# Kernel tuning notes

Hardware: AMD Instinct MI355X
Metric: run time of the kernel (lower is better)

## Reference

```python
import jax, jax.numpy as jnp
import numpy as np

N = 50000      # nodes
F_IN = 500     # in_channels
MID = 64       # mid_layer_channel
H = 2          # heads
OUT = 40       # out_channels
E = 800000     # edges per order
ORDER = 3
NEG_SLOPE = 0.2


def _gat(x, edge_index, W, a_src, a_dst, b, concat):
    # PyG-style GATConv (eval mode, dropout off), with self loops.
    n = x.shape[0]
    heads, ch = a_src.shape
    h = (x @ W).reshape(n, heads, ch)                    # [N,H,C]
    loop = jnp.arange(n)
    src = jnp.concatenate([edge_index[0], loop])
    dst = jnp.concatenate([edge_index[1], loop])
    al_s = jnp.sum(h * a_src, axis=-1)                   # [N,H]
    al_d = jnp.sum(h * a_dst, axis=-1)                   # [N,H]
    e = jax.nn.leaky_relu(al_s[src] + al_d[dst], NEG_SLOPE)   # [Etot,H]
    m = jax.ops.segment_max(e, dst, num_segments=n)      # softmax over incoming edges per dst
    ex = jnp.exp(e - m[dst])
    den = jax.ops.segment_sum(ex, dst, num_segments=n)
    alpha = ex / (den[dst] + 1e-16)
    out = jax.ops.segment_sum(alpha[:, :, None] * h[src], dst, num_segments=n)  # [N,H,C]
    if concat:
        return out.reshape(n, heads * ch) + b
    return out.mean(axis=1) + b


def _aggr(states, Wmix, wfin):
    # NOrderAggrConv (depth=2): mix order states with [order,order] weights + ELU,
    # then reduce to a single state with a learned [order] combination.
    h = jnp.stack(states, axis=1)                        # [N,order,C]
    h = jax.nn.elu(jnp.einsum('nkc,kj->njc', h, Wmix))
    return jnp.einsum('nkc,k->nc', h, wfin)


def setup_inputs():
    key = jax.random.key(0)
    ks = jax.random.split(key, 40)
    d = {}
    d['node_feature'] = jax.random.normal(ks[0], (N, F_IN), jnp.float32)
    for o in range(ORDER):
        d[f'adj{o}'] = jax.random.randint(ks[1 + o], (2, E), 0, N)
    i = 4
    s = 0.05
    layer_dims = [(F_IN, MID, H * MID), (MID * H, OUT, OUT)]
    for l, (fin, c, bdim) in enumerate(layer_dims):
        for o in range(ORDER):
            d[f'W_{l}_{o}'] = jax.random.normal(ks[i], (fin, H * c), jnp.float32) * s; i += 1
            d[f'as_{l}_{o}'] = jax.random.normal(ks[i], (H, c), jnp.float32) * s; i += 1
            d[f'ad_{l}_{o}'] = jax.random.normal(ks[i], (H, c), jnp.float32) * s; i += 1
            d[f'b_{l}_{o}'] = jnp.zeros((bdim,), jnp.float32)
    for l in range(2):
        d[f'agg{l}_W'] = jax.random.normal(ks[i], (ORDER, ORDER), jnp.float32) * 0.5; i += 1
        d[f'agg{l}_w'] = jnp.full((ORDER,), 1.0 / ORDER, jnp.float32)
    return d


def reference(node_feature, adj0, adj1, adj2,
              W_0_0, as_0_0, ad_0_0, b_0_0,
              W_0_1, as_0_1, ad_0_1, b_0_1,
              W_0_2, as_0_2, ad_0_2, b_0_2,
              W_1_0, as_1_0, ad_1_0, b_1_0,
              W_1_1, as_1_1, ad_1_1, b_1_1,
              W_1_2, as_1_2, ad_1_2, b_1_2,
              agg0_W, agg0_w, agg1_W, agg1_w):
    adjs = (adj0, adj1, adj2)
    p0 = ((W_0_0, as_0_0, ad_0_0, b_0_0),
          (W_0_1, as_0_1, ad_0_1, b_0_1),
          (W_0_2, as_0_2, ad_0_2, b_0_2))
    p1 = ((W_1_0, as_1_0, ad_1_0, b_1_0),
          (W_1_1, as_1_1, ad_1_1, b_1_1),
          (W_1_2, as_1_2, ad_1_2, b_1_2))
    aggs = ((agg0_W, agg0_w), (agg1_W, agg1_w))
    x = node_feature  # eval mode: dropout is identity
    for l, params in enumerate((p0, p1)):
        concat = (l == 0)
        states = [jax.nn.elu(_gat(x, adjs[o], *params[o], concat)) for o in range(ORDER)]
        x = _aggr(states, *aggs[l])
    return jax.nn.log_softmax(x, axis=1)
```

## Files before the change

kernel.cpp:

```cpp
#include <hip/hip_runtime.h>
#include <cstdint>
#include <cstddef>
#include <math.h>


typedef __attribute__((ext_vector_type(8))) short short8;
typedef __attribute__((ext_vector_type(4))) float f32x4;
typedef __attribute__((ext_vector_type(2))) float f32x2;

struct P3f { const float* p[3]; };
struct P3c { const int* p[3]; };

__device__ __forceinline__ float leakyf(float x) { return x > 0.f ? x : 0.2f * x; }
__device__ __forceinline__ float eluf(float x)   { return x > 0.f ? x : expm1f(x); }

__device__ __forceinline__ unsigned short bf16r(float x) {
  unsigned int u = __float_as_uint(x);
  u += 0x7fffu + ((u >> 16) & 1u);
  return (unsigned short)(u >> 16);
}
__device__ __forceinline__ float bflo(unsigned int u) { return __uint_as_float(u << 16); }
__device__ __forceinline__ float bfhi(unsigned int u) { return __uint_as_float(u & 0xffff0000u); }

__device__ __forceinline__ void bf8_fma2(uint4 q, float xx, f32x2* a) {
  f32x2 v0 = {bflo(q.x), bfhi(q.x)};
  f32x2 v1 = {bflo(q.y), bfhi(q.y)};
  f32x2 v2 = {bflo(q.z), bfhi(q.z)};
  f32x2 v3 = {bflo(q.w), bfhi(q.w)};
  a[0] += xx * v0;
  a[1] += xx * v1;
  a[2] += xx * v2;
  a[3] += xx * v3;
}

__global__ __launch_bounds__(256) void zero_int_kernel(int* p, int n) {
  int i = blockIdx.x * blockDim.x + threadIdx.x;
  if (i < n) p[i] = 0;
}

__global__ __launch_bounds__(256) void convA_kernel(const float* __restrict__ A,
    unsigned short* __restrict__ Ab, int M, int K, int Kpad) {
  int i = blockIdx.x * blockDim.x + threadIdx.x;
  int row = i >> 6;
  int koff = (i & 63) * 8;
  if (row >= M) return;
  const float* ap = A + (size_t)row * K;
  unsigned short v[8];
  if (koff + 8 <= K) {
    float4 q0 = ((const float4*)(ap + koff))[0];
    float4 q1 = ((const float4*)(ap + koff))[1];
    v[0] = bf16r(q0.x); v[1] = bf16r(q0.y); v[2] = bf16r(q0.z); v[3] = bf16r(q0.w);
    v[4] = bf16r(q1.x); v[5] = bf16r(q1.y); v[6] = bf16r(q1.z); v[7] = bf16r(q1.w);
  } else {
#pragma unroll
    for (int k = 0; k < 8; ++k)
      v[k] = (koff + k < K) ? bf16r(ap[koff + k]) : (unsigned short)0;
  }
  *(uint4*)(Ab + (size_t)row * Kpad + koff) = *(const uint4*)v;
}

__global__ __launch_bounds__(256) void count3_kernel(P3c adj, int* __restrict__ cntb,
    int* __restrict__ posb, int E, int N) {
  int i = blockIdx.x * blockDim.x + threadIdx.x;
  int o = blockIdx.y;
  if (i < E) {
    int d = adj.p[o][E + i];
    posb[(size_t)o * E + i] = atomicAdd(&cntb[o * N + d], 1);
  }
}

#define SCAN_T 256
#define SCAN_VPT 8
#define SCAN_TILE 2048

__global__ __launch_bounds__(SCAN_T) void scan1_kernel(const int* __restrict__ cntb,
    int* __restrict__ rowptrb, int* __restrict__ bsums, int N) {
  __shared__ int lds[SCAN_T];
  const int o = blockIdx.y;
  const int* cnt = cntb + o * N;
  int* rowptr = rowptrb + o * (N + 1);
  int t = threadIdx.x;
  int base = blockIdx.x * SCAN_TILE + t * SCAN_VPT;
  int v[SCAN_VPT];
  int s = 0;
#pragma unroll
  for (int i = 0; i < SCAN_VPT; ++i) {
    int idx = base + i;
    int x = (idx < N) ? cnt[idx] : 0;
    s += x;
    v[i] = s;
  }
  lds[t] = s;
  __syncthreads();
  for (int off = 1; off < SCAN_T; off <<= 1) {
    int add = (t >= off) ? lds[t - off] : 0;
    __syncthreads();
    lds[t] += add;
    __syncthreads();
  }
  int excl = (t > 0) ? lds[t - 1] : 0;
#pragma unroll
  for (int i = 0; i < SCAN_VPT; ++i) {
    int idx = base + i;
    if (idx < N) rowptr[idx + 1] = excl + v[i];
  }
  if (t == SCAN_T - 1) bsums[o * 64 + blockIdx.x] = lds[t];
}

__global__ void scan2_kernel(int* bsums, int nb, int* rowptrb, int N) {
  if (threadIdx.x == 0 && blockIdx.x == 0) {
    for (int o = 0; o < 3; ++o) {
      int run = 0;
      for (int i = 0; i < nb; ++i) {
        int x = bsums[o * 64 + i];
        bsums[o * 64 + i] = run;
        run += x;
      }
      rowptrb[o * (N + 1)] = 0;
    }
  }
}

__global__ __launch_bounds__(256) void scan3_kernel(int* __restrict__ rowptrb,
    const int* __restrict__ bsums, int N) {
  int idx = blockIdx.x * blockDim.x + threadIdx.x;
  int o = blockIdx.y;
  if (idx < N) rowptrb[o * (N + 1) + idx + 1] += bsums[o * 64 + idx / SCAN_TILE];
}

__global__ __launch_bounds__(256) void fill3_kernel(P3c adj,
    const int* __restrict__ rowptrb, const int* __restrict__ posb,
    int* __restrict__ colvb, int E, int N) {
  int i = blockIdx.x * blockDim.x + threadIdx.x;
  int o = blockIdx.y;
  if (i < E) {
    const int* a = adj.p[o];
    int d = a[E + i];
    int pos = posb[(size_t)o * E + i];
    colvb[(size_t)o * E + rowptrb[o * (N + 1) + d] + pos] = a[i];
  }
}

__global__ __launch_bounds__(256) void alpha3_kernel(const int* __restrict__ rowptrB,
    const int* __restrict__ colvB, const float2* __restrict__ alsB,
    const float2* __restrict__ aldB, float2* __restrict__ alphB, int N, int E) {
  int w = blockIdx.x * blockDim.x + threadIdx.x;
  int o = blockIdx.y;
  if (w >= N) return;
  const int* rowptr = rowptrB + o * (N + 1);
  const int* colv = colvB + (size_t)o * E;
  const float2* als = alsB + (size_t)o * N;
  const float2 b = (aldB + (size_t)o * N)[w];
  float2* alph = alphB + (size_t)o * E;
  const int beg = rowptr[w], end = rowptr[w + 1];
  for (int j = beg; j < end; ++j) {
    int s = colv[j];
    float2 a = als[s];
    alph[j] = make_float2(__expf(leakyf(a.x + b.x)), __expf(leakyf(a.y + b.y)));
  }
}

__global__ __launch_bounds__(256) void conv_bt3_kernel(P3f W,
    unsigned short* __restrict__ BtB, int K, int NC, int Kpad) {
  int n = blockIdx.y;
  int o = blockIdx.z;
  int k = blockIdx.x * 256 + threadIdx.x;
  if (k >= Kpad) return;
  float v = (k < K) ? W.p[o][(size_t)k * NC + n] : 0.f;
  BtB[(size_t)o * NC * Kpad + (size_t)n * Kpad + k] = bf16r(v);
}

#define GBM 128
#define LDSTRIDE 40

template<int NT>
__device__ __forceinline__ void gemm_body(int m0, int o, int t,
    const unsigned short* __restrict__ Ab, const unsigned short* __restrict__ BtB,
    P3f asp, P3f adp, unsigned short* __restrict__ CbB,
    float2* __restrict__ alsB, float2* __restrict__ aldB, int M, int Kpad,
    unsigned short* As, unsigned short* Bs) {
  constexpr int NC = NT * 16;
  constexpr int CH = NT * 8;
  const int wave = t >> 6, lane = t & 63;
  const int quad = lane >> 4, l16 = lane & 15;
  const unsigned short* Bt = BtB + (size_t)o * NC * Kpad;
  unsigned short* Cb = CbB + (size_t)o * M * NC;
  float2* al_s = alsB + (size_t)o * M;
  float2* al_d = aldB + (size_t)o * M;
  const float* a_src = asp.p[o];
  const float* a_dst = adp.p[o];

  f32x4 acc[2][NT];
#pragma unroll
  for (int i = 0; i < 2; ++i)
#pragma unroll
    for (int j = 0; j < NT; ++j) acc[i][j] = (f32x4){0.f, 0.f, 0.f, 0.f};

  const int arow = t >> 1;
  const int akoff = (t & 1) * 16;
  const int gm = m0 + arow;
  const unsigned short* arowp = Ab + (size_t)gm * Kpad;
  const unsigned short* browp = Bt + (size_t)arow * Kpad;

  for (int k0 = 0; k0 < Kpad; k0 += 32) {
    if (k0) __syncthreads();
    const int kb = k0 + akoff;
    {
      uint4 q0 = {0, 0, 0, 0}, q1 = {0, 0, 0, 0};
      if (gm < M) {
        const uint4* p = (const uint4*)(arowp + kb);
        q0 = p[0]; q1 = p[1];
      }
      short8* dst = (short8*)&As[arow * LDSTRIDE + akoff];
      union { uint4 q; short8 s; } c0, c1;
      c0.q = q0; c1.q = q1;
      dst[0] = c0.s;
      dst[1] = c1.s;
    }
    if (arow < NC) {
      const uint4* p = (const uint4*)(browp + kb);
      uint4 q0 = p[0], q1 = p[1];
      short8* dst = (short8*)&Bs[arow * LDSTRIDE + akoff];
      union { uint4 q; short8 s; } c0, c1;
      c0.q = q0; c1.q = q1;
      dst[0] = c0.s;
      dst[1] = c1.s;
    }
    __syncthreads();
    short8 af[2];
#pragma unroll
    for (int rt = 0; rt < 2; ++rt)
      af[rt] = *(const short8*)&As[(wave * 32 + rt * 16 + l16) * LDSTRIDE + quad * 8];
    short8 bfv[NT];
#pragma unroll
    for (int ct = 0; ct < NT; ++ct)
      bfv[ct] = *(const short8*)&Bs[(ct * 16 + l16) * LDSTRIDE + quad * 8];
#pragma unroll
    for (int rt = 0; rt < 2; ++rt)
#pragma unroll
      for (int ct = 0; ct < NT; ++ct)
        acc[rt][ct] = __builtin_amdgcn_mfma_f32_16x16x32_bf16(af[rt], bfv[ct],
                                                              acc[rt][ct], 0, 0, 0);
  }
  float asv[NT], adv[NT];
#pragma unroll
  for (int ct = 0; ct < NT; ++ct) {
    int col = ct * 16 + l16;
    asv[ct] = a_src[col];
    adv[ct] = a_dst[col];
  }
#pragma unroll
  for (int rt = 0; rt < 2; ++rt) {
    int gr0 = m0 + wave * 32 + rt * 16 + quad * 4;
#pragma unroll
    for (int r = 0; r < 4; ++r) {
      int gr = gr0 + r;
      float ps0 = 0.f, ps1 = 0.f, pd0 = 0.f, pd1 = 0.f;
#pragma unroll
      for (int ct = 0; ct < NT; ++ct) {
        int col = ct * 16 + l16;
        float v = acc[rt][ct][r];
        if (gr < M) Cb[(size_t)gr * NC + col] = bf16r(v);
        if (col < CH) { ps0 += v * asv[ct]; pd0 += v * adv[ct]; }
        else          { ps1 += v * asv[ct]; pd1 += v * adv[ct]; }
      }
#pragma unroll
      for (int off = 1; off < 16; off <<= 1) {
        ps0 += __shfl_xor(ps0, off, 64);
        ps1 += __shfl_xor(ps1, off, 64);
        pd0 += __shfl_xor(pd0, off, 64);
        pd1 += __shfl_xor(pd1, off, 64);
      }
      if (l16 == 0 && gr < M) {
        al_s[gr] = make_float2(ps0, ps1);
        al_d[gr] = make_float2(pd0, pd1);
      }
    }
  }
}

template<int NT>
__global__ __launch_bounds__(256) void mfma_gemm_kernel(
    const unsigned short* __restrict__ Ab, const unsigned short* __restrict__ BtB,
    P3f asp, P3f adp, unsigned short* __restrict__ CbB,
    float2* __restrict__ alsB, float2* __restrict__ aldB, int M, int Kpad) {
  __shared__ unsigned short As[GBM * LDSTRIDE];
  __shared__ unsigned short Bs[NT * 16 * LDSTRIDE];
  gemm_body<NT>(blockIdx.x * GBM, blockIdx.y, threadIdx.x,
                Ab, BtB, asp, adp, CbB, alsB, aldB, M, Kpad, As, Bs);
}

__global__ __launch_bounds__(256) void gemm0_count_kernel(
    const unsigned short* __restrict__ Ab, const unsigned short* __restrict__ BtB,
    P3f asp, P3f adp, unsigned short* __restrict__ CbB,
    float2* __restrict__ alsB, float2* __restrict__ aldB, int M, int Kpad,
    P3c adj, int* __restrict__ cntb, int* __restrict__ posb, int E, int N,
    int nbG) {
  __shared__ unsigned short As[GBM * LDSTRIDE];
  __shared__ unsigned short Bs[128 * LDSTRIDE];
  const int x = blockIdx.x;
  const int o = blockIdx.y;
  const int gx = x / 9;
  const int rem = x - gx * 9;
  if (rem == 0 && gx < nbG) {
    gemm_body<8>(gx * GBM, o, threadIdx.x,
                 Ab, BtB, asp, adp, CbB, alsB, aldB, M, Kpad, As, Bs);
  } else {
    int nG = (x + 8) / 9;
    if (nG > nbG) nG = nbG;
    const int c = x - nG;
    const int i = c * 256 + threadIdx.x;
    if (i < E) {
      int d = adj.p[o][E + i];
      posb[(size_t)o * E + i] = atomicAdd(&cntb[o * N + d], 1);
    }
  }
}

template<int C, int CONCAT>
__global__ __launch_bounds__(256) void gat_slot4_kernel(
    const unsigned short* __restrict__ hB, const float2* __restrict__ alsB,
    const float2* __restrict__ aldB, const int* __restrict__ rowptrB,
    const int* __restrict__ colvB, const float2* __restrict__ alphB,
    P3f biasp, unsigned short* __restrict__ outB, int N, int E) {
  constexpr int HC = 2 * C;
  constexpr int FLd = HC / 8;
  constexpr int HB = C / 8;
  constexpr int OW = CONCAT ? HC : C;
  const int o = blockIdx.y;
  const unsigned short* h = hB + (size_t)o * N * HC;
  const float2* al_s = alsB + (size_t)o * N;
  const float2* al_d = aldB + (size_t)o * N;
  const int* rowptr = rowptrB + o * (N + 1);
  const int* colv = colvB + (size_t)o * E;
  const float2* alph = alphB + (size_t)o * E;
  const float* bias = biasp.p[o];
  unsigned short* out = outB + (size_t)o * N * OW;

  const int gw = (blockIdx.x * blockDim.x + threadIdx.x) >> 6;
  const int lane = threadIdx.x & 63;
  const int slot = lane >> 4;
  const int f4 = lane & 15;
  const int w = gw * 4 + slot;
  if (gw * 4 >= N) return;
  const bool vn = w < N;
  const int wc = vn ? w : N - 1;
  const bool hl = f4 < FLd;

  const int beg = rowptr[wc];
  const int deg = vn ? (rowptr[wc + 1] - beg) : 0;
  int md = deg;
  md = max(md, __shfl_xor(md, 32, 64));
  md = max(md, __shfl_xor(md, 16, 64));

  const float2 ad = al_d[wc];
  const float2 asf = al_s[wc];
  const float xs0 = __expf(leakyf(asf.x + ad.x));
  const float xs1 = __expf(leakyf(asf.y + ad.y));
  float dp0 = xs0, dp1 = xs1;

  f32x2 acc[4] = {}, acc2[4] = {};
  if (hl) {
    uint4 q = ((const uint4*)(h + (size_t)wc * HC))[f4];
    bf8_fma2(q, (f4 < HB) ? xs0 : xs1, acc);
  }

  const float2 z2 = make_float2(0.f, 0.f);
  for (int t = 0; t < md; t += 4) {
    const int j0 = beg + t;
    const bool v0 = t < deg;
    const bool v1 = t + 1 < deg;
    const bool v2 = t + 2 < deg;
    const bool v3 = t + 3 < deg;
    const int s0 = v0 ? colv[j0] : 0;
    const int s1 = v1 ? colv[j0 + 1] : 0;
    const int s2 = v2 ? colv[j0 + 2] : 0;
    const int s3 = v3 ? colv[j0 + 3] : 0;
    const float2 a0 = v0 ? alph[j0] : z2;
    const float2 a1 = v1 ? alph[j0 + 1] : z2;
    const float2 a2 = v2 ? alph[j0 + 2] : z2;
    const float2 a3 = v3 ? alph[j0 + 3] : z2;
    uint4 q0 = make_uint4(0, 0, 0, 0), q1 = q0, q2 = q0, q3 = q0;
    if (v0 && hl) q0 = ((const uint4*)(h + (size_t)s0 * HC))[f4];
    if (v1 && hl) q1 = ((const uint4*)(h + (size_t)s1 * HC))[f4];
    if (v2 && hl) q2 = ((const uint4*)(h + (size_t)s2 * HC))[f4];
    if (v3 && hl) q3 = ((const uint4*)(h + (size_t)s3 * HC))[f4];
    dp0 += (a0.x + a1.x) + (a2.x + a3.x);
    dp1 += (a0.y + a1.y) + (a2.y + a3.y);
    if (v0 && hl) bf8_fma2(q0, (f4 < HB) ? a0.x : a0.y, acc);
    if (v1 && hl) bf8_fma2(q1, (f4 < HB) ? a1.x : a1.y, acc2);
    if (v2 && hl) bf8_fma2(q2, (f4 < HB) ? a2.x : a2.y, acc);
    if (v3 && hl) bf8_fma2(q3, (f4 < HB) ? a3.x : a3.y, acc2);
  }
#pragma unroll
  for (int i = 0; i < 4; ++i) acc[i] += acc2[i];

  const float inv0 = 1.f / (dp0 + 1e-16f), inv1 = 1.f / (dp1 + 1e-16f);
  if (CONCAT) {
    if (vn && hl) {
      const float xx = (f4 < HB) ? inv0 : inv1;
      const float* bp = bias + f4 * 8;
      unsigned int pk[4];
#pragma unroll
      for (int i = 0; i < 4; ++i) {
        unsigned short lo = bf16r(eluf(acc[i][0] * xx + bp[2 * i]));
        unsigned short hi = bf16r(eluf(acc[i][1] * xx + bp[2 * i + 1]));
        pk[i] = (unsigned int)lo | ((unsigned int)hi << 16);
      }
      ((uint4*)(out + (size_t)w * OW + f4 * 8))[0] = make_uint4(pk[0], pk[1], pk[2], pk[3]);
    }
  } else {
    float p[8];
#pragma unroll
    for (int i = 0; i < 4; ++i) {
      p[2 * i]     = __shfl(acc[i][0], lane + HB, 64);
      p[2 * i + 1] = __shfl(acc[i][1], lane + HB, 64);
    }
    if (vn && f4 < HB) {
      const float* bp = bias + f4 * 8;
      unsigned int pk[4];
#pragma unroll
      for (int i = 0; i < 4; ++i) {
        float v0 = 0.5f * (acc[i][0] * inv0 + p[2 * i] * inv1) + bp[2 * i];
        float v1 = 0.5f * (acc[i][1] * inv0 + p[2 * i + 1] * inv1) + bp[2 * i + 1];
        pk[i] = (unsigned int)bf16r(eluf(v0)) | ((unsigned int)bf16r(eluf(v1)) << 16);
      }
      ((uint4*)(out + (size_t)w * OW + f4 * 8))[0] = make_uint4(pk[0], pk[1], pk[2], pk[3]);
    }
  }
}

template<int BF16OUT>
__global__ __launch_bounds__(256) void mixb_kernel(const unsigned short* __restrict__ sb,
    const float* __restrict__ Wm, const float* __restrict__ wf,
    void* __restrict__ out, int perU) {
  int i = blockIdx.x * blockDim.x + threadIdx.x;
  if (i >= perU) return;
  const unsigned int* sp = (const unsigned int*)sb;
  unsigned int u0 = sp[i];
  unsigned int u1 = sp[perU + i];
  unsigned int u2 = sp[2 * perU + i];
  float a0 = bflo(u0), a1 = bfhi(u0);
  float b0 = bflo(u1), b1 = bfhi(u1);
  float c0 = bflo(u2), c1 = bfhi(u2);
  float r0 = 0.f, r1 = 0.f;
#pragma unroll
  for (int j = 0; j < 3; ++j) {
    float w0 = Wm[j], w1 = Wm[3 + j], w2 = Wm[6 + j], wj = wf[j];
    r0 += wj * eluf(a0 * w0 + b0 * w1 + c0 * w2);
    r1 += wj * eluf(a1 * w0 + b1 * w1 + c1 * w2);
  }
  if (BF16OUT) {
    ((unsigned int*)out)[i] = (unsigned int)bf16r(r0) | ((unsigned int)bf16r(r1) << 16);
  } else {
    ((float2*)out)[i] = make_float2(r0, r1);
  }
}

__global__ __launch_bounds__(256) void log_softmax_kernel(const float* __restrict__ x,
    float* __restrict__ out, int N, int C) {
  int w = (blockIdx.x * blockDim.x + threadIdx.x) >> 6;
  int lane = threadIdx.x & 63;
  if (w >= N) return;
  float v = (lane < C) ? x[(size_t)w * C + lane] : -INFINITY;
  float mx = v;
#pragma unroll
  for (int off = 1; off < 64; off <<= 1) mx = fmaxf(mx, __shfl_xor(mx, off, 64));
  float ex = (lane < C) ? expf(v - mx) : 0.f;
  float s = ex;
#pragma unroll
  for (int off = 1; off < 64; off <<= 1) s += __shfl_xor(s, off, 64);
  if (lane < C) out[(size_t)w * C + lane] = v - mx - logf(s);
}

extern "C" void kernel_launch(void* const* d_in, const int* in_sizes, int n_in,
                              void* d_out, int out_size, void* d_ws, size_t ws_size,
                              hipStream_t stream) {
  const int F_IN = 500;
  const int N = in_sizes[0] / F_IN;
  const int E = in_sizes[1] / 2;
  const int HC0 = 128;
  const int HC1 = 80;
  const int C1 = 40;
  const int K0pad = 512, K1pad = 128;

  const float* x0 = (const float*)d_in[0];
  P3c adj;
  adj.p[0] = (const int*)d_in[1];
  adj.p[1] = (const int*)d_in[2];
  adj.p[2] = (const int*)d_in[3];
  P3f W0p, as0p, ad0p, b0p, W1p, as1p, ad1p, b1p;
  for (int o = 0; o < 3; ++o) {
    W0p.p[o]  = (const float*)d_in[4 + 4 * o + 0];
    as0p.p[o] = (const float*)d_in[4 + 4 * o + 1];
    ad0p.p[o] = (const float*)d_in[4 + 4 * o + 2];
    b0p.p[o]  = (const float*)d_in[4 + 4 * o + 3];
    W1p.p[o]  = (const float*)d_in[16 + 4 * o + 0];
    as1p.p[o] = (const float*)d_in[16 + 4 * o + 1];
    ad1p.p[o] = (const float*)d_in[16 + 4 * o + 2];
    b1p.p[o]  = (const float*)d_in[16 + 4 * o + 3];
  }
  const float* agg0W = (const float*)d_in[28];
  const float* agg0w = (const float*)d_in[29];
  const float* agg1W = (const float*)d_in[30];
  const float* agg1w = (const float*)d_in[31];

  char* ws = (char*)d_ws;
  size_t off = 0;
  auto alloc = [&](size_t bytes) -> void* {
    off = (off + 255) & ~(size_t)255;
    void* p = ws + off;
    off += bytes;
    return p;
  };
  int* rowptrb = (int*)alloc((size_t)3 * (N + 1) * 4);
  int* colvb   = (int*)alloc((size_t)3 * E * 4);
  int* cntb    = (int*)alloc((size_t)3 * N * 4);
  int* bsums   = (int*)alloc(3 * 64 * 4);
  unsigned short* x0b = (unsigned short*)alloc((size_t)N * K0pad * 2);
  unsigned short* hB  = (unsigned short*)alloc((size_t)3 * N * HC0 * 2);
  unsigned short* stB = (unsigned short*)alloc((size_t)3 * N * HC0 * 2);
  float* x2 = (float*)alloc((size_t)N * C1 * 4);
  float2* alsB = (float2*)alloc((size_t)3 * N * 8);
  float2* aldB = (float2*)alloc((size_t)3 * N * 8);
  unsigned short* Bt0B = (unsigned short*)alloc((size_t)3 * HC0 * K0pad * 2);
  unsigned short* Bt1B = (unsigned short*)alloc((size_t)3 * HC1 * K1pad * 2);
  float2* alphb = (float2*)x0b;
  int* posb = (int*)stB;
  (void)ws_size;

  const int TB = 256;
  const int nbE = (E + TB - 1) / TB;
  const int nbN = (N + TB - 1) / TB;
  const int scanBlocks = (N + SCAN_TILE - 1) / SCAN_TILE;
  const int gemmBlocks = (N + GBM - 1) / GBM;
  const int slot4Blocks = (int)(((size_t)((N + 3) / 4) * 64 + TB - 1) / TB);
  const int lsBlocks = (int)(((size_t)N * 64 + TB - 1) / TB);

  convA_kernel<<<(int)(((size_t)N * 64 + TB - 1) / TB), TB, 0, stream>>>(
      x0, x0b, N, F_IN, K0pad);
  conv_bt3_kernel<<<dim3((K0pad + 255) / 256, HC0, 3), TB, 0, stream>>>(W0p, Bt0B, F_IN, HC0, K0pad);
  conv_bt3_kernel<<<dim3((K1pad + 255) / 256, HC1, 3), TB, 0, stream>>>(W1p, Bt1B, HC0, HC1, K1pad);

  zero_int_kernel<<<(3 * N + TB - 1) / TB, TB, 0, stream>>>(cntb, 3 * N);
  if (8 * gemmBlocks >= nbE) {
    gemm0_count_kernel<<<dim3(gemmBlocks * 9, 3), TB, 0, stream>>>(
        x0b, Bt0B, as0p, ad0p, hB, alsB, aldB, N, K0pad,
        adj, cntb, posb, E, N, gemmBlocks);
  } else {
    count3_kernel<<<dim3(nbE, 3), TB, 0, stream>>>(adj, cntb, posb, E, N);
    mfma_gemm_kernel<8><<<dim3(gemmBlocks, 3), TB, 0, stream>>>(
        x0b, Bt0B, as0p, ad0p, hB, alsB, aldB, N, K0pad);
  }

  scan1_kernel<<<dim3(scanBlocks, 3), SCAN_T, 0, stream>>>(cntb, rowptrb, bsums, N);
  scan2_kernel<<<1, 64, 0, stream>>>(bsums, scanBlocks, rowptrb, N);
  scan3_kernel<<<dim3(nbN, 3), TB, 0, stream>>>(rowptrb, bsums, N);
  fill3_kernel<<<dim3(nbE, 3), TB, 0, stream>>>(adj, rowptrb, posb, colvb, E, N);

  alpha3_kernel<<<dim3(nbN, 3), TB, 0, stream>>>(rowptrb, colvb, alsB, aldB, alphb, N, E);
  gat_slot4_kernel<64, 1><<<dim3(slot4Blocks, 3), TB, 0, stream>>>(
      hB, alsB, aldB, rowptrb, colvb, alphb, b0p, stB, N, E);
  mixb_kernel<1><<<((N * HC0 / 2) + TB - 1) / TB, TB, 0, stream>>>(
      stB, agg0W, agg0w, stB, N * HC0 / 2);

  mfma_gemm_kernel<5><<<dim3(gemmBlocks, 3), TB, 0, stream>>>(
      stB, Bt1B, as1p, ad1p, hB, alsB, aldB, N, K1pad);
  alpha3_kernel<<<dim3(nbN, 3), TB, 0, stream>>>(rowptrb, colvb, alsB, aldB, alphb, N, E);
  gat_slot4_kernel<40, 0><<<dim3(slot4Blocks, 3), TB, 0, stream>>>(
      hB, alsB, aldB, rowptrb, colvb, alphb, b1p, stB, N, E);
  mixb_kernel<0><<<((N * C1 / 2) + TB - 1) / TB, TB, 0, stream>>>(
      stB, agg1W, agg1w, x2, N * C1 / 2);

  log_softmax_kernel<<<lsBlocks, TB, 0, stream>>>(x2, (float*)d_out, N, C1);
}
```

Before: 760.3 us.

## Fuse three-order GAT aggregation with order mixing and log-softmax

The GAT aggregation kernel now loops over all three orders inside one thread group, keeps the per-order ELU outputs in registers, and applies the NOrderAggr mix directly. For the second layer it also computes log-softmax in-kernel via shuffles and writes the final output. This removes the separate mix and log_softmax launches and the bf16 round-trip of the three per-order state tensors. The cost is a grid that is a third the size, with each wave doing three sequential gathers, which lowers parallelism and raises register pressure. The layer-0 output written to stB still aliases the posb buffer.

Result: slower. 806.2 us (+6.0%).

```diff
diff --git a/kernel.cpp b/kernel.cpp
--- a/kernel.cpp
+++ b/kernel.cpp
@@ -318,25 +318,15 @@
 }
 
 template<int C, int CONCAT>
-__global__ __launch_bounds__(256) void gat_slot4_kernel(
+__global__ __launch_bounds__(256) void gat3_kernel(
     const unsigned short* __restrict__ hB, const float2* __restrict__ alsB,
     const float2* __restrict__ aldB, const int* __restrict__ rowptrB,
     const int* __restrict__ colvB, const float2* __restrict__ alphB,
-    P3f biasp, unsigned short* __restrict__ outB, int N, int E) {
+    P3f biasp, const float* __restrict__ Wm, const float* __restrict__ wf,
+    void* __restrict__ outp, int N, int E) {
   constexpr int HC = 2 * C;
   constexpr int FLd = HC / 8;
   constexpr int HB = C / 8;
-  constexpr int OW = CONCAT ? HC : C;
-  const int o = blockIdx.y;
-  const unsigned short* h = hB + (size_t)o * N * HC;
-  const float2* al_s = alsB + (size_t)o * N;
-  const float2* al_d = aldB + (size_t)o * N;
-  const int* rowptr = rowptrB + o * (N + 1);
-  const int* colv = colvB + (size_t)o * E;
-  const float2* alph = alphB + (size_t)o * E;
-  const float* bias = biasp.p[o];
-  unsigned short* out = outB + (size_t)o * N * OW;
-
   const int gw = (blockIdx.x * blockDim.x + threadIdx.x) >> 6;
   const int lane = threadIdx.x & 63;
   const int slot = lane >> 4;
@@ -347,130 +337,146 @@
   const int wc = vn ? w : N - 1;
   const bool hl = f4 < FLd;
 
-  const int beg = rowptr[wc];
-  const int deg = vn ? (rowptr[wc + 1] - beg) : 0;
-  int md = deg;
-  md = max(md, __shfl_xor(md, 32, 64));
-  md = max(md, __shfl_xor(md, 16, 64));
-
-  const float2 ad = al_d[wc];
-  const float2 asf = al_s[wc];
-  const float xs0 = __expf(leakyf(asf.x + ad.x));
-  const float xs1 = __expf(leakyf(asf.y + ad.y));
-  float dp0 = xs0, dp1 = xs1;
-
-  f32x2 acc[4] = {}, acc2[4] = {};
-  if (hl) {
-    uint4 q = ((const uint4*)(h + (size_t)wc * HC))[f4];
-    bf8_fma2(q, (f4 < HB) ? xs0 : xs1, acc);
-  }
-
-  const float2 z2 = make_float2(0.f, 0.f);
-  for (int t = 0; t < md; t += 4) {
-    const int j0 = beg + t;
-    const bool v0 = t < deg;
-    const bool v1 = t + 1 < deg;
-    const bool v2 = t + 2 < deg;
-    const bool v3 = t + 3 < deg;
-    const int s0 = v0 ? colv[j0] : 0;
-    const int s1 = v1 ? colv[j0 + 1] : 0;
-    const int s2 = v2 ? colv[j0 + 2] : 0;
-    const int s3 = v3 ? colv[j0 + 3] : 0;
-    const float2 a0 = v0 ? alph[j0] : z2;
-    const float2 a1 = v1 ? alph[j0 + 1] : z2;
-    const float2 a2 = v2 ? alph[j0 + 2] : z2;
-    const float2 a3 = v3 ? alph[j0 + 3] : z2;
-    uint4 q0 = make_uint4(0, 0, 0, 0), q1 = q0, q2 = q0, q3 = q0;
-    if (v0 && hl) q0 = ((const uint4*)(h + (size_t)s0 * HC))[f4];
-    if (v1 && hl) q1 = ((const uint4*)(h + (size_t)s1 * HC))[f4];
-    if (v2 && hl) q2 = ((const uint4*)(h + (size_t)s2 * HC))[f4];
-    if (v3 && hl) q3 = ((const uint4*)(h + (size_t)s3 * HC))[f4];
-    dp0 += (a0.x + a1.x) + (a2.x + a3.x);
-    dp1 += (a0.y + a1.y) + (a2.y + a3.y);
-    if (v0 && hl) bf8_fma2(q0, (f4 < HB) ? a0.x : a0.y, acc);
-    if (v1 && hl) bf8_fma2(q1, (f4 < HB) ? a1.x : a1.y, acc2);
-    if (v2 && hl) bf8_fma2(q2, (f4 < HB) ? a2.x : a2.y, acc);
-    if (v3 && hl) bf8_fma2(q3, (f4 < HB) ? a3.x : a3.y, acc2);
-  }
-#pragma unroll
-  for (int i = 0; i < 4; ++i) acc[i] += acc2[i];
-
-  const float inv0 = 1.f / (dp0 + 1e-16f), inv1 = 1.f / (dp1 + 1e-16f);
+  f32x2 st[3][4] = {};
+
+#pragma unroll
+  for (int o = 0; o < 3; ++o) {
+    const unsigned short* h = hB + (size_t)o * N * HC;
+    const float2* al_s = alsB + (size_t)o * N;
+    const float2* al_d = aldB + (size_t)o * N;
+    const int* rowptr = rowptrB + o * (N + 1);
+    const int* colv = colvB + (size_t)o * E;
+    const float2* alph = alphB + (size_t)o * E;
+    const float* bias = biasp.p[o];
+
+    const int beg = rowptr[wc];
+    const int deg = vn ? (rowptr[wc + 1] - beg) : 0;
+    int md = deg;
+    md = max(md, __shfl_xor(md, 32, 64));
+    md = max(md, __shfl_xor(md, 16, 64));
+
+    const float2 ad = al_d[wc];
+    const float2 asf = al_s[wc];
+    const float xs0 = __expf(leakyf(asf.x + ad.x));
+    const float xs1 = __expf(leakyf(asf.y + ad.y));
+    float dp0 = xs0, dp1 = xs1;
+
+    f32x2 acc[4] = {}, acc2[4] = {};
+    if (hl) {
+      uint4 q = ((const uint4*)(h + (size_t)wc * HC))[f4];
+      bf8_fma2(q, (f4 < HB) ? xs0 : xs1, acc);
+    }
+
+    const float2 z2 = make_float2(0.f, 0.f);
+    for (int t = 0; t < md; t += 4) {
+      const int j0 = beg + t;
+      const bool v0 = t < deg;
+      const bool v1 = t + 1 < deg;
+      const bool v2 = t + 2 < deg;
+      const bool v3 = t + 3 < deg;
+      const int s0 = v0 ? colv[j0] : 0;
+      const int s1 = v1 ? colv[j0 + 1] : 0;
+      const int s2 = v2 ? colv[j0 + 2] : 0;
+      const int s3 = v3 ? colv[j0 + 3] : 0;
+      const float2 a0 = v0 ? alph[j0] : z2;
+      const float2 a1 = v1 ? alph[j0 + 1] : z2;
+      const float2 a2 = v2 ? alph[j0 + 2] : z2;
+      const float2 a3 = v3 ? alph[j0 + 3] : z2;
+      uint4 q0 = make_uint4(0, 0, 0, 0), q1 = q0, q2 = q0, q3 = q0;
+      if (v0 && hl) q0 = ((const uint4*)(h + (size_t)s0 * HC))[f4];
+      if (v1 && hl) q1 = ((const uint4*)(h + (size_t)s1 * HC))[f4];
+      if (v2 && hl) q2 = ((const uint4*)(h + (size_t)s2 * HC))[f4];
+      if (v3 && hl) q3 = ((const uint4*)(h + (size_t)s3 * HC))[f4];
+      dp0 += (a0.x + a1.x) + (a2.x + a3.x);
+      dp1 += (a0.y + a1.y) + (a2.y + a3.y);
+      if (v0 && hl) bf8_fma2(q0, (f4 < HB) ? a0.x : a0.y, acc);
+      if (v1 && hl) bf8_fma2(q1, (f4 < HB) ? a1.x : a1.y, acc2);
+      if (v2 && hl) bf8_fma2(q2, (f4 < HB) ? a2.x : a2.y, acc);
+      if (v3 && hl) bf8_fma2(q3, (f4 < HB) ? a3.x : a3.y, acc2);
+    }
+#pragma unroll
+    for (int i = 0; i < 4; ++i) acc[i] += acc2[i];
+
+    const float inv0 = 1.f / (dp0 + 1e-16f), inv1 = 1.f / (dp1 + 1e-16f);
+    if (CONCAT) {
+      if (hl) {
+        const float xx = (f4 < HB) ? inv0 : inv1;
+        const float* bp = bias + f4 * 8;
+#pragma unroll
+        for (int i = 0; i < 4; ++i) {
+          st[o][i][0] = eluf(acc[i][0] * xx + bp[2 * i]);
+          st[o][i][1] = eluf(acc[i][1] * xx + bp[2 * i + 1]);
+        }
+      }
+    } else {
+      float p[8];
+#pragma unroll
+      for (int i = 0; i < 4; ++i) {
+        p[2 * i]     = __shfl(acc[i][0], lane + HB, 64);
+        p[2 * i + 1] = __shfl(acc[i][1], lane + HB, 64);
+      }
+      if (f4 < HB) {
+        const float* bp = bias + f4 * 8;
+#pragma unroll
+        for (int i = 0; i < 4; ++i) {
+          st[o][i][0] = eluf(0.5f * (acc[i][0] * inv0 + p[2 * i] * inv1) + bp[2 * i]);
+          st[o][i][1] = eluf(0.5f * (acc[i][1] * inv0 + p[2 * i + 1] * inv1) + bp[2 * i + 1]);
+        }
+      }
+    }
+  }
+
+  f32x2 r[4];
+#pragma unroll
+  for (int i = 0; i < 4; ++i) {
+#pragma unroll
+    for (int c = 0; c < 2; ++c) {
+      const float a = st[0][i][c], b = st[1][i][c], d = st[2][i][c];
+      float m = 0.f;
+#pragma unroll
+      for (int j = 0; j < 3; ++j)
+        m += wf[j] * eluf(a * Wm[j] + b * Wm[3 + j] + d * Wm[6 + j]);
+      r[i][c] = m;
+    }
+  }
+
   if (CONCAT) {
     if (vn && hl) {
-      const float xx = (f4 < HB) ? inv0 : inv1;
-      const float* bp = bias + f4 * 8;
       unsigned int pk[4];
 #pragma unroll
-      for (int i = 0; i < 4; ++i) {
-        unsigned short lo = bf16r(eluf(acc[i][0] * xx + bp[2 * i]));
-        unsigned short hi = bf16r(eluf(acc[i][1] * xx + bp[2 * i + 1]));
-        pk[i] = (unsigned int)lo | ((unsigned int)hi << 16);
-      }
-      ((uint4*)(out + (size_t)w * OW + f4 * 8))[0] = make_uint4(pk[0], pk[1], pk[2], pk[3]);
+      for (int i = 0; i < 4; ++i)
+        pk[i] = (unsigned int)bf16r(r[i][0]) | ((unsigned int)bf16r(r[i][1]) << 16);
+      ((uint4*)((unsigned short*)outp + (size_t)w * HC + f4 * 8))[0] =
+          make_uint4(pk[0], pk[1], pk[2], pk[3]);
     }
   } else {
-    float p[8];
-#pragma unroll
-    for (int i = 0; i < 4; ++i) {
-      p[2 * i]     = __shfl(acc[i][0], lane + HB, 64);
-      p[2 * i + 1] = __shfl(acc[i][1], lane + HB, 64);
-    }
-    if (vn && f4 < HB) {
-      const float* bp = bias + f4 * 8;
-      unsigned int pk[4];
-#pragma unroll
-      for (int i = 0; i < 4; ++i) {
-        float v0 = 0.5f * (acc[i][0] * inv0 + p[2 * i] * inv1) + bp[2 * i];
-        float v1 = 0.5f * (acc[i][1] * inv0 + p[2 * i + 1] * inv1) + bp[2 * i + 1];
-        pk[i] = (unsigned int)bf16r(eluf(v0)) | ((unsigned int)bf16r(eluf(v1)) << 16);
-      }
-      ((uint4*)(out + (size_t)w * OW + f4 * 8))[0] = make_uint4(pk[0], pk[1], pk[2], pk[3]);
-    }
-  }
-}
-
-template<int BF16OUT>
-__global__ __launch_bounds__(256) void mixb_kernel(const unsigned short* __restrict__ sb,
-    const float* __restrict__ Wm, const float* __restrict__ wf,
-    void* __restrict__ out, int perU) {
-  int i = blockIdx.x * blockDim.x + threadIdx.x;
-  if (i >= perU) return;
-  const unsigned int* sp = (const unsigned int*)sb;
-  unsigned int u0 = sp[i];
-  unsigned int u1 = sp[perU + i];
-  unsigned int u2 = sp[2 * perU + i];
-  float a0 = bflo(u0), a1 = bfhi(u0);
-  float b0 = bflo(u1), b1 = bfhi(u1);
-  float c0 = bflo(u2), c1 = bfhi(u2);
-  float r0 = 0.f, r1 = 0.f;
-#pragma unroll
-  for (int j = 0; j < 3; ++j) {
-    float w0 = Wm[j], w1 = Wm[3 + j], w2 = Wm[6 + j], wj = wf[j];
-    r0 += wj * eluf(a0 * w0 + b0 * w1 + c0 * w2);
-    r1 += wj * eluf(a1 * w0 + b1 * w1 + c1 * w2);
-  }
-  if (BF16OUT) {
-    ((unsigned int*)out)[i] = (unsigned int)bf16r(r0) | ((unsigned int)bf16r(r1) << 16);
-  } else {
-    ((float2*)out)[i] = make_float2(r0, r1);
-  }
-}
-
-__global__ __launch_bounds__(256) void log_softmax_kernel(const float* __restrict__ x,
-    float* __restrict__ out, int N, int C) {
-  int w = (blockIdx.x * blockDim.x + threadIdx.x) >> 6;
-  int lane = threadIdx.x & 63;
-  if (w >= N) return;
-  float v = (lane < C) ? x[(size_t)w * C + lane] : -INFINITY;
-  float mx = v;
-#pragma unroll
-  for (int off = 1; off < 64; off <<= 1) mx = fmaxf(mx, __shfl_xor(mx, off, 64));
-  float ex = (lane < C) ? expf(v - mx) : 0.f;
-  float s = ex;
-#pragma unroll
-  for (int off = 1; off < 64; off <<= 1) s += __shfl_xor(s, off, 64);
-  if (lane < C) out[(size_t)w * C + lane] = v - mx - logf(s);
+    const bool act = vn && (f4 < HB);
+    float lm = -INFINITY;
+    if (act) {
+#pragma unroll
+      for (int i = 0; i < 4; ++i) lm = fmaxf(lm, fmaxf(r[i][0], r[i][1]));
+    }
+    const int sb = slot << 4;
+    float m = lm;
+#pragma unroll
+    for (int k = 0; k < HB; ++k) m = fmaxf(m, __shfl(lm, sb + k, 64));
+    float ls = 0.f;
+    if (act) {
+#pragma unroll
+      for (int i = 0; i < 4; ++i) ls += expf(r[i][0] - m) + expf(r[i][1] - m);
+    }
+    float s = 0.f;
+#pragma unroll
+    for (int k = 0; k < HB; ++k) s += __shfl(ls, sb + k, 64);
+    if (act) {
+      const float lse = logf(s);
+      float* op = (float*)outp + (size_t)w * 40 + f4 * 8;
+      ((float4*)op)[0] = make_float4(r[0][0] - m - lse, r[0][1] - m - lse,
+                                     r[1][0] - m - lse, r[1][1] - m - lse);
+      ((float4*)op)[1] = make_float4(r[2][0] - m - lse, r[2][1] - m - lse,
+                                     r[3][0] - m - lse, r[3][1] - m - lse);
+    }
+  }
 }
 
 extern "C" void kernel_launch(void* const* d_in, const int* in_sizes, int n_in,
@@ -481,7 +487,6 @@
   const int E = in_sizes[1] / 2;
   const int HC0 = 128;
   const int HC1 = 80;
-  const int C1 = 40;
   const int K0pad = 512, K1pad = 128;
 
   const float* x0 = (const float*)d_in[0];
@@ -520,7 +525,6 @@
   unsigned short* x0b = (unsigned short*)alloc((size_t)N * K0pad * 2);
   unsigned short* hB  = (unsigned short*)alloc((size_t)3 * N * HC0 * 2);
   unsigned short* stB = (unsigned short*)alloc((size_t)3 * N * HC0 * 2);
-  float* x2 = (float*)alloc((size_t)N * C1 * 4);
   float2* alsB = (float2*)alloc((size_t)3 * N * 8);
   float2* aldB = (float2*)alloc((size_t)3 * N * 8);
   unsigned short* Bt0B = (unsigned short*)alloc((size_t)3 * HC0 * K0pad * 2);
@@ -535,7 +539,6 @@
   const int scanBlocks = (N + SCAN_TILE - 1) / SCAN_TILE;
   const int gemmBlocks = (N + GBM - 1) / GBM;
   const int slot4Blocks = (int)(((size_t)((N + 3) / 4) * 64 + TB - 1) / TB);
-  const int lsBlocks = (int)(((size_t)N * 64 + TB - 1) / TB);
 
   convA_kernel<<<(int)(((size_t)N * 64 + TB - 1) / TB), TB, 0, stream>>>(
       x0, x0b, N, F_IN, K0pad);
@@ -559,18 +562,12 @@
   fill3_kernel<<<dim3(nbE, 3), TB, 0, stream>>>(adj, rowptrb, posb, colvb, E, N);
 
   alpha3_kernel<<<dim3(nbN, 3), TB, 0, stream>>>(rowptrb, colvb, alsB, aldB, alphb, N, E);
-  gat_slot4_kernel<64, 1><<<dim3(slot4Blocks, 3), TB, 0, stream>>>(
-      hB, alsB, aldB, rowptrb, colvb, alphb, b0p, stB, N, E);
-  mixb_kernel<1><<<((N * HC0 / 2) + TB - 1) / TB, TB, 0, stream>>>(
-      stB, agg0W, agg0w, stB, N * HC0 / 2);
+  gat3_kernel<64, 1><<<slot4Blocks, TB, 0, stream>>>(
+      hB, alsB, aldB, rowptrb, colvb, alphb, b0p, agg0W, agg0w, stB, N, E);
 
   mfma_gemm_kernel<5><<<dim3(gemmBlocks, 3), TB, 0, stream>>>(
       stB, Bt1B, as1p, ad1p, hB, alsB, aldB, N, K1pad);
   alpha3_kernel<<<dim3(nbN, 3), TB, 0, stream>>>(rowptrb, colvb, alsB, aldB, alphb, N, E);
-  gat_slot4_kernel<40, 0><<<dim3(slot4Blocks, 3), TB, 0, stream>>>(
-      hB, alsB, aldB, rowptrb, colvb, alphb, b1p, stB, N, E);
-  mixb_kernel<0><<<((N * C1 / 2) + TB - 1) / TB, TB, 0, stream>>>(
-      stB, agg1W, agg1w, x2, N * C1 / 2);
-
-  log_softmax_kernel<<<lsBlocks, TB, 0, stream>>>(x2, (float*)d_out, N, C1);
-}
+  gat3_kernel<40, 0><<<slot4Blocks, TB, 0, stream>>>(
+      hB, alsB, aldB, rowptrb, colvb, alphb, b1p, agg1W, agg1w, d_out, N, E);
+}
```
